# Kernel optimization log

Measured on AMD Instinct MI355X. Metric: run time of the kernel, lower is better.

Reference implementation:

```python
import jax, jax.numpy as jnp
import numpy as np

B, FIN, FOUT, FH = 32, 32, 32, 64
H = W = 128
LAT = 512
K_IN, K_MID, K_OUT, K_SHORT = FH * FIN, FH * FH, FOUT * FH, FOUT * FIN
K_TOTAL = K_IN + K_MID + K_OUT + K_SHORT + FH + FH + FOUT + FOUT  # 9408


def setup_inputs() -> dict:
    key = jax.random.key(0)
    ks = jax.random.split(key, 20)
    def rn(k, shape, scale=None):
        s = scale if scale is not None else 1.0 / np.sqrt(shape[-1])
        return jax.random.normal(k, shape, dtype=jnp.float32) * s
    return {
        "x": jax.random.normal(ks[0], (B, FIN, H, W), dtype=jnp.float32),
        "lat": jax.random.normal(ks[1], (B, LAT), dtype=jnp.float32),
        "w0": rn(ks[2], (LAT, LAT)), "b0": rn(ks[3], (LAT,), 0.02),
        "w1a": rn(ks[4], (2 * LAT, LAT)), "b1a": rn(ks[5], (2 * LAT,), 0.02),
        "w1b": rn(ks[6], (LAT, 2 * LAT)), "b1b": rn(ks[7], (LAT,), 0.02),
        "w1s": rn(ks[8], (LAT, LAT)), "b1s": rn(ks[9], (LAT,), 0.02),
        "w2a": rn(ks[10], (2 * LAT, LAT)), "b2a": rn(ks[11], (2 * LAT,), 0.02),
        "w2b": rn(ks[12], (K_TOTAL, 2 * LAT)), "b2b": rn(ks[13], (K_TOTAL,), 0.02),
        "w2s": rn(ks[14], (K_TOTAL, LAT)), "b2s": rn(ks[15], (K_TOTAL,), 0.02),
        "wfa": rn(ks[16], (K_TOTAL, K_TOTAL)), "bfa": rn(ks[17], (K_TOTAL,), 0.02),
    }


def _lrb(h, wa, ba, wb, bb, ws, bs):
    # LinearResidualBlock: shortcut + 2-layer MLP with ReLU
    return h @ ws.T + bs + jax.nn.relu(h @ wa.T + ba) @ wb.T + bb


def reference(x, lat, w0, b0, w1a, b1a, w1b, b1b, w1s, b1s,
              w2a, b2a, w2b, b2b, w2s, b2s, wfa, bfa):
    # hypernetwork: dyna_k then LinearFA (forward is a plain linear)
    h = lat @ w0.T + b0                              # [B, 512]
    h = _lrb(h, w1a, b1a, w1b, b1b, w1s, b1s)        # [B, 512]
    h = _lrb(h, w2a, b2a, w2b, b2b, w2s, b2s)        # [B, K_TOTAL]
    ks = h @ wfa.T + bfa                             # [B, K_TOTAL]

    sizes = [K_IN, K_MID, K_OUT, K_SHORT, FH, FH, FOUT, FOUT]
    offs = np.cumsum([0] + sizes)
    k_in = ks[:, offs[0]:offs[1]].reshape(B, FH, FIN)
    k_mid = ks[:, offs[1]:offs[2]].reshape(B, FH, FH)
    k_out = ks[:, offs[2]:offs[3]].reshape(B, FOUT, FH)
    k_short = ks[:, offs[3]:offs[4]].reshape(B, FOUT, FIN)
    b_in = ks[:, offs[4]:offs[5]][:, :, None, None]    # [B, FH, 1, 1]
    b_mid = ks[:, offs[5]:offs[6]][:, :, None, None]
    b_out = ks[:, offs[6]:offs[7]][:, :, None, None]   # [B, FOUT, 1, 1]
    b_short = ks[:, offs[7]:offs[8]][:, :, None, None]

    # per-sample 1x1 grouped convs == batched matmuls over channels
    xs = jnp.einsum('bihw,boi->bohw', x, k_short) + b_short
    xn = jax.nn.relu(jnp.einsum('bihw,boi->bohw', x, k_in) + b_in)
    xn = jax.nn.relu(jnp.einsum('bihw,boi->bohw', xn, k_mid) + b_mid)
    xn = jnp.einsum('bihw,boi->bohw', xn, k_out) + b_out
    return xn + xs
```

## Files before the change

### kernel.cpp

```cpp
#include <hip/hip_runtime.h>
#include <cstdint>

#define KT 9408
#define NT 256
#define KC 16

__global__ __launch_bounds__(256, 1) void gemm32_partial(
    const float* __restrict__ X1, const float* __restrict__ W1, int K1,
    const float* __restrict__ X2, const float* __restrict__ W2, int K2,
    float* __restrict__ partial, int O, int ksplit)
{
    __shared__ float Xs[KC][32];
    __shared__ float Wt[KC][NT];

    const int t      = threadIdx.x;
    const int o0     = blockIdx.x * NT;
    const int s      = blockIdx.y;
    const int kchunk = (K1 + K2) / ksplit;
    const int kbeg   = s * kchunk;
    const int kend   = kbeg + kchunk;
    const int lane   = t & 63;
    const int wv     = t >> 6;

    const int sr  = t >> 2;
    const int sc4 = (t & 3) << 2;

    float4 wpre[4];
    float  xpre[2];

    {
        int kc0 = kbeg;
#pragma unroll
        for (int p = 0; p < 4; ++p) {
            int r = sr + 64 * p;
            int o = o0 + r;
            int kg = kc0 + sc4;
            float4 v = make_float4(0.f, 0.f, 0.f, 0.f);
            if (o < O)
                v = (kg < K1) ? *(const float4*)&W1[(size_t)o * K1 + kg]
                              : *(const float4*)&W2[(size_t)o * K2 + (kg - K1)];
            wpre[p] = v;
        }
#pragma unroll
        for (int it = 0; it < 2; ++it) {
            int idx = t + 256 * it;
            int kg  = kc0 + (idx >> 5);
            int bb  = idx & 31;
            xpre[it] = (kg < K1) ? X1[(size_t)bb * K1 + kg]
                                 : X2[(size_t)bb * K2 + (kg - K1)];
        }
    }

    float acc[8][4];
#pragma unroll
    for (int bi = 0; bi < 8; bi++)
#pragma unroll
        for (int j = 0; j < 4; j++) acc[bi][j] = 0.f;

    for (int kc0 = kbeg; kc0 < kend; kc0 += KC) {
#pragma unroll
        for (int it = 0; it < 2; ++it) {
            int idx = t + 256 * it;
            Xs[idx >> 5][idx & 31] = xpre[it];
        }
#pragma unroll
        for (int p = 0; p < 4; ++p) {
            int r = sr + 64 * p;
            Wt[sc4 + 0][r] = wpre[p].x;
            Wt[sc4 + 1][r] = wpre[p].y;
            Wt[sc4 + 2][r] = wpre[p].z;
            Wt[sc4 + 3][r] = wpre[p].w;
        }
        __syncthreads();

        if (kc0 + KC < kend) {
            int kn = kc0 + KC;
#pragma unroll
            for (int p = 0; p < 4; ++p) {
                int r = sr + 64 * p;
                int o = o0 + r;
                int kg = kn + sc4;
                float4 v = make_float4(0.f, 0.f, 0.f, 0.f);
                if (o < O)
                    v = (kg < K1) ? *(const float4*)&W1[(size_t)o * K1 + kg]
                                  : *(const float4*)&W2[(size_t)o * K2 + (kg - K1)];
                wpre[p] = v;
            }
#pragma unroll
            for (int it = 0; it < 2; ++it) {
                int idx = t + 256 * it;
                int kg  = kn + (idx >> 5);
                int bb  = idx & 31;
                xpre[it] = (kg < K1) ? X1[(size_t)bb * K1 + kg]
                                     : X2[(size_t)bb * K2 + (kg - K1)];
            }
        }

#pragma unroll
        for (int c = 0; c < KC; c++) {
            float4 xa = *(const float4*)&Xs[c][wv * 8];
            float4 xb = *(const float4*)&Xs[c][wv * 8 + 4];
            float xv[8] = {xa.x, xa.y, xa.z, xa.w, xb.x, xb.y, xb.z, xb.w};
            float w[4];
#pragma unroll
            for (int j = 0; j < 4; j++) w[j] = Wt[c][lane + 64 * j];
#pragma unroll
            for (int bi = 0; bi < 8; bi++)
#pragma unroll
                for (int j = 0; j < 4; j++) acc[bi][j] += xv[bi] * w[j];
        }
        __syncthreads();
    }

#pragma unroll
    for (int bi = 0; bi < 8; bi++) {
        int b = wv * 8 + bi;
#pragma unroll
        for (int j = 0; j < 4; j++) {
            int o = o0 + lane + 64 * j;
            if (o < O)
                partial[((size_t)s * 32 + b) * O + o] = acc[bi][j];
        }
    }
}

__global__ __launch_bounds__(256) void reduce_bias(
    const float* __restrict__ partial, const float* __restrict__ bias1,
    const float* __restrict__ bias2, float* __restrict__ Y, int O, int relu,
    int ksplit)
{
    int idx = blockIdx.x * 256 + threadIdx.x;
    if (idx >= 32 * O) return;
    int b = idx / O, o = idx - b * O;
    float s = bias1[o] + (bias2 ? bias2[o] : 0.f);
    for (int k = 0; k < ksplit; k++)
        s += partial[((size_t)k * 32 + b) * O + o];
    Y[idx] = relu ? fmaxf(s, 0.f) : s;
}

typedef __attribute__((ext_vector_type(8))) short bf16x8;
typedef __attribute__((ext_vector_type(4))) float f32x4;

__device__ inline uint32_t pkbf(float lo, float hi) {
    uint32_t a = __builtin_bit_cast(uint32_t, lo);
    uint32_t b = __builtin_bit_cast(uint32_t, hi);
    a = (a + 0x7FFFu + ((a >> 16) & 1u)) >> 16;
    b = (b + 0x7FFFu + ((b >> 16) & 1u)) & 0xFFFF0000u;
    return a | b;
}

#define MFMA16(a, b, c) __builtin_amdgcn_mfma_f32_16x16x32_bf16(a, b, c, 0, 0, 0)

#define TPW 16

__global__ __launch_bounds__(256, 3) void conv_mfma(
    const float* __restrict__ x, const float* __restrict__ ks,
    float* __restrict__ out)
{
    const int t  = threadIdx.x;
    const int b  = blockIdx.y;
    const int l  = t & 63;
    const int g  = l >> 4;
    const int n  = l & 15;
    const int wid = blockIdx.x * 4 + (t >> 6);

    const float* __restrict__ kb = ks + (size_t)b * KT;

    auto loadA = [&](const float* W, int ldw, int row0, int k0) -> bf16x8 {
        const float* p = W + (size_t)(row0 + n) * ldw + k0 + 4 * g;
        float4 lo = *(const float4*)p;
        float4 hi = *(const float4*)(p + 16);
        union { bf16x8 v; uint32_t u[4]; } r;
        r.u[0] = pkbf(lo.x, lo.y);
        r.u[1] = pkbf(lo.z, lo.w);
        r.u[2] = pkbf(hi.x, hi.y);
        r.u[3] = pkbf(hi.z, hi.w);
        return r.v;
    };
    auto loadBias = [&](int off) -> f32x4 {
        float4 v = *(const float4*)&kb[off + 4 * g];
        f32x4 r; r[0] = v.x; r[1] = v.y; r[2] = v.z; r[3] = v.w;
        return r;
    };

    bf16x8 ain[4], amid[4][2], aout[2][2], ashort[2];
#pragma unroll
    for (int rt = 0; rt < 4; ++rt) ain[rt] = loadA(kb, 32, 16 * rt, 0);
#pragma unroll
    for (int ot = 0; ot < 4; ++ot)
#pragma unroll
        for (int kf = 0; kf < 2; ++kf) amid[ot][kf] = loadA(kb + 2048, 64, 16 * ot, 32 * kf);
#pragma unroll
    for (int ot = 0; ot < 2; ++ot)
#pragma unroll
        for (int kf = 0; kf < 2; ++kf) aout[ot][kf] = loadA(kb + 6144, 64, 16 * ot, 32 * kf);
#pragma unroll
    for (int ot = 0; ot < 2; ++ot) ashort[ot] = loadA(kb + 8192, 32, 16 * ot, 0);

    f32x4 bin[4], bmid[4], bos[2];
#pragma unroll
    for (int rt = 0; rt < 4; ++rt) bin[rt] = loadBias(9216 + 16 * rt);
#pragma unroll
    for (int ot = 0; ot < 4; ++ot) bmid[ot] = loadBias(9280 + 16 * ot);
#pragma unroll
    for (int ot = 0; ot < 2; ++ot) {
        f32x4 a = loadBias(9344 + 16 * ot);
        f32x4 c = loadBias(9376 + 16 * ot);
#pragma unroll
        for (int r = 0; r < 4; ++r) a[r] += c[r];
        bos[ot] = a;
    }

    const float* __restrict__ xbase = x + (size_t)b * 524288 + (size_t)(4 * g) * 16384 + n;
    float* __restrict__ obase = out + (size_t)b * 524288 + (size_t)(4 * g) * 16384 + n;

#pragma unroll 1
    for (int it = 0; it < TPW; ++it) {
        const int px0 = (wid * TPW + it) * 16;

        const float* p = xbase + px0;
        float e0 = p[0], e1 = p[16384], e2 = p[2 * 16384], e3 = p[3 * 16384];
        const float* q = p + (size_t)16 * 16384;
        float e4 = q[0], e5 = q[16384], e6 = q[2 * 16384], e7 = q[3 * 16384];
        union { bf16x8 v; uint32_t u[4]; } bx;
        bx.u[0] = pkbf(e0, e1); bx.u[1] = pkbf(e2, e3);
        bx.u[2] = pkbf(e4, e5); bx.u[3] = pkbf(e6, e7);

        f32x4 h[4];
#pragma unroll
        for (int rt = 0; rt < 4; ++rt) {
            f32x4 acc = MFMA16(ain[rt], bx.v, bin[rt]);
#pragma unroll
            for (int r = 0; r < 4; ++r) acc[r] = fmaxf(acc[r], 0.f);
            h[rt] = acc;
        }
        union { bf16x8 v; uint32_t u[4]; } hb0, hb1;
        hb0.u[0] = pkbf(h[0][0], h[0][1]); hb0.u[1] = pkbf(h[0][2], h[0][3]);
        hb0.u[2] = pkbf(h[1][0], h[1][1]); hb0.u[3] = pkbf(h[1][2], h[1][3]);
        hb1.u[0] = pkbf(h[2][0], h[2][1]); hb1.u[1] = pkbf(h[2][2], h[2][3]);
        hb1.u[2] = pkbf(h[3][0], h[3][1]); hb1.u[3] = pkbf(h[3][2], h[3][3]);

        f32x4 m[4];
#pragma unroll
        for (int ot = 0; ot < 4; ++ot) {
            f32x4 acc = MFMA16(amid[ot][0], hb0.v, bmid[ot]);
            acc = MFMA16(amid[ot][1], hb1.v, acc);
#pragma unroll
            for (int r = 0; r < 4; ++r) acc[r] = fmaxf(acc[r], 0.f);
            m[ot] = acc;
        }
        union { bf16x8 v; uint32_t u[4]; } mb0, mb1;
        mb0.u[0] = pkbf(m[0][0], m[0][1]); mb0.u[1] = pkbf(m[0][2], m[0][3]);
        mb0.u[2] = pkbf(m[1][0], m[1][1]); mb0.u[3] = pkbf(m[1][2], m[1][3]);
        mb1.u[0] = pkbf(m[2][0], m[2][1]); mb1.u[1] = pkbf(m[2][2], m[2][3]);
        mb1.u[2] = pkbf(m[3][0], m[3][1]); mb1.u[3] = pkbf(m[3][2], m[3][3]);

#pragma unroll
        for (int ot = 0; ot < 2; ++ot) {
            f32x4 acc = MFMA16(ashort[ot], bx.v, bos[ot]);
            acc = MFMA16(aout[ot][0], mb0.v, acc);
            acc = MFMA16(aout[ot][1], mb1.v, acc);
            float* po = obase + (size_t)(16 * ot) * 16384 + px0;
            po[0]         = acc[0];
            po[16384]     = acc[1];
            po[2 * 16384] = acc[2];
            po[3 * 16384] = acc[3];
        }
    }
}

extern "C" void kernel_launch(void* const* d_in, const int* in_sizes, int n_in,
                              void* d_out, int out_size, void* d_ws, size_t ws_size,
                              hipStream_t stream)
{
    const float* x   = (const float*)d_in[0];
    const float* lat = (const float*)d_in[1];
    const float* w0  = (const float*)d_in[2];
    const float* b0  = (const float*)d_in[3];
    const float* w1a = (const float*)d_in[4];
    const float* b1a = (const float*)d_in[5];
    const float* w1b = (const float*)d_in[6];
    const float* b1b = (const float*)d_in[7];
    const float* w1s = (const float*)d_in[8];
    const float* b1s = (const float*)d_in[9];
    const float* w2a = (const float*)d_in[10];
    const float* b2a = (const float*)d_in[11];
    const float* w2b = (const float*)d_in[12];
    const float* b2b = (const float*)d_in[13];
    const float* w2s = (const float*)d_in[14];
    const float* b2s = (const float*)d_in[15];
    const float* wfa = (const float*)d_in[16];
    const float* bfa = (const float*)d_in[17];

    float* ws  = (float*)d_ws;
    float* h0  = ws;
    float* t1  = ws + 16384;
    float* h1  = ws + 49152;
    float* t2  = ws + 65536;
    float* h2  = ws + 98304;
    float* ksb = ws + 399360;
    float* pbuf = (float*)d_out;

    dim3 blk(256);
    auto g  = [](int O, int ks) { return dim3((unsigned)((O + NT - 1) / NT), (unsigned)ks); };
    auto rg = [](int O) { return dim3((unsigned)((32 * O + 255) / 256)); };

    gemm32_partial<<<g(512, 32), blk, 0, stream>>>(lat, w0, 512, nullptr, nullptr, 0, pbuf, 512, 32);
    reduce_bias<<<rg(512), blk, 0, stream>>>(pbuf, b0, nullptr, h0, 512, 0, 32);
    gemm32_partial<<<g(1024, 32), blk, 0, stream>>>(h0, w1a, 512, nullptr, nullptr, 0, pbuf, 1024, 32);
    reduce_bias<<<rg(1024), blk, 0, stream>>>(pbuf, b1a, nullptr, t1, 1024, 1, 32);
    gemm32_partial<<<g(512, 32), blk, 0, stream>>>(h0, w1s, 512, t1, w1b, 1024, pbuf, 512, 32);
    reduce_bias<<<rg(512), blk, 0, stream>>>(pbuf, b1s, b1b, h1, 512, 0, 32);
    gemm32_partial<<<g(1024, 32), blk, 0, stream>>>(h1, w2a, 512, nullptr, nullptr, 0, pbuf, 1024, 32);
    reduce_bias<<<rg(1024), blk, 0, stream>>>(pbuf, b2a, nullptr, t2, 1024, 1, 32);
    gemm32_partial<<<g(KT, 32), blk, 0, stream>>>(h1, w2s, 512, t2, w2b, 1024, pbuf, KT, 32);
    reduce_bias<<<rg(KT), blk, 0, stream>>>(pbuf, b2s, b2b, h2, KT, 0, 32);
    gemm32_partial<<<g(KT, 28), blk, 0, stream>>>(h2, wfa, KT, nullptr, nullptr, 0, pbuf, KT, 28);
    reduce_bias<<<rg(KT), blk, 0, stream>>>(pbuf, bfa, nullptr, ksb, KT, 0, 28);

    conv_mfma<<<dim3(16, 32), blk, 0, stream>>>(x, ksb, (float*)d_out);
}
```

Baseline: 293.8 us.

## Replace split-K plus reduce with fused small-GEMM kernel for hypernet layers

Adds a smallgemm kernel that splits K across the four waves of one block, reduces in shared memory, and applies bias and ReLU in-kernel. This replaces the split-K gemm32_partial plus reduce_bias pairs for the first five linear layers, removing five launches and the partial-buffer round trips. The large wfa GEMM keeps the split-K path but moves from 28 to 21 splits. The small kernels launch few blocks for the 512/1024-wide layers and do not double-buffer their loads, so latency hiding may be weaker.

```diff
diff --git a/kernel.cpp b/kernel.cpp
--- a/kernel.cpp
+++ b/kernel.cpp
@@ -5,9 +5,82 @@
 #define NT 256
 #define KC 16
 
+__global__ __launch_bounds__(256) void smallgemm(
+    const float* __restrict__ X1, const float* __restrict__ W1, int K1,
+    const float* __restrict__ X2, const float* __restrict__ W2, int K2,
+    const float* __restrict__ bias1, const float* __restrict__ bias2,
+    float* __restrict__ Y, int O, int relu)
+{
+    __shared__ float Xs[4][KC][32];
+    __shared__ float Wt[4][KC][16];
+    __shared__ float red[4][16][32];
+
+    const int t    = threadIdx.x;
+    const int lane = t & 63;
+    const int w    = t >> 6;
+    const int o0   = blockIdx.x * 16;
+    const int o_l  = lane & 15;
+    const int bg   = lane >> 4;
+    const int Kq   = (K1 + K2) >> 2;
+    const int kbeg = w * Kq;
+    const int kend = kbeg + Kq;
+
+    const int wr  = lane >> 2;
+    const int wc4 = (lane & 3) << 2;
+
+    float acc[8];
+#pragma unroll
+    for (int i = 0; i < 8; ++i) acc[i] = 0.f;
+
+    for (int kc = kbeg; kc < kend; kc += KC) {
+#pragma unroll
+        for (int i = 0; i < 8; ++i) {
+            int idx = lane + 64 * i;
+            int c   = idx >> 5;
+            int bb  = idx & 31;
+            int kg  = kc + c;
+            Xs[w][c][bb] = (kg < K1) ? X1[(size_t)bb * K1 + kg]
+                                     : X2[(size_t)bb * K2 + (kg - K1)];
+        }
+        {
+            int kg = kc + wc4;
+            float4 v = (kg < K1) ? *(const float4*)&W1[(size_t)(o0 + wr) * K1 + kg]
+                                 : *(const float4*)&W2[(size_t)(o0 + wr) * K2 + (kg - K1)];
+            Wt[w][wc4 + 0][wr] = v.x;
+            Wt[w][wc4 + 1][wr] = v.y;
+            Wt[w][wc4 + 2][wr] = v.z;
+            Wt[w][wc4 + 3][wr] = v.w;
+        }
+#pragma unroll
+        for (int c = 0; c < KC; ++c) {
+            float wv = Wt[w][c][o_l];
+            float4 xa = *(const float4*)&Xs[w][c][8 * bg];
+            float4 xb = *(const float4*)&Xs[w][c][8 * bg + 4];
+            acc[0] += wv * xa.x; acc[1] += wv * xa.y;
+            acc[2] += wv * xa.z; acc[3] += wv * xa.w;
+            acc[4] += wv * xb.x; acc[5] += wv * xb.y;
+            acc[6] += wv * xb.z; acc[7] += wv * xb.w;
+        }
+    }
+
+#pragma unroll
+    for (int bi = 0; bi < 8; ++bi) red[w][o_l][8 * bg + bi] = acc[bi];
+    __syncthreads();
+
+#pragma unroll
+    for (int half = 0; half < 2; ++half) {
+        int cell = t + 256 * half;
+        int o = cell >> 5;
+        int b = cell & 31;
+        float s = red[0][o][b] + red[1][o][b] + red[2][o][b] + red[3][o][b];
+        s += bias1[o0 + o] + (bias2 ? bias2[o0 + o] : 0.f);
+        if (relu) s = fmaxf(s, 0.f);
+        Y[(size_t)b * O + o0 + o] = s;
+    }
+}
+
 __global__ __launch_bounds__(256, 1) void gemm32_partial(
     const float* __restrict__ X1, const float* __restrict__ W1, int K1,
-    const float* __restrict__ X2, const float* __restrict__ W2, int K2,
     float* __restrict__ partial, int O, int ksplit)
 {
     __shared__ float Xs[KC][32];
@@ -16,7 +89,7 @@
     const int t      = threadIdx.x;
     const int o0     = blockIdx.x * NT;
     const int s      = blockIdx.y;
-    const int kchunk = (K1 + K2) / ksplit;
+    const int kchunk = K1 / ksplit;
     const int kbeg   = s * kchunk;
     const int kend   = kbeg + kchunk;
     const int lane   = t & 63;
@@ -34,20 +107,14 @@
         for (int p = 0; p < 4; ++p) {
             int r = sr + 64 * p;
             int o = o0 + r;
-            int kg = kc0 + sc4;
             float4 v = make_float4(0.f, 0.f, 0.f, 0.f);
-            if (o < O)
-                v = (kg < K1) ? *(const float4*)&W1[(size_t)o * K1 + kg]
-                              : *(const float4*)&W2[(size_t)o * K2 + (kg - K1)];
+            if (o < O) v = *(const float4*)&W1[(size_t)o * K1 + kc0 + sc4];
             wpre[p] = v;
         }
 #pragma unroll
         for (int it = 0; it < 2; ++it) {
             int idx = t + 256 * it;
-            int kg  = kc0 + (idx >> 5);
-            int bb  = idx & 31;
-            xpre[it] = (kg < K1) ? X1[(size_t)bb * K1 + kg]
-                                 : X2[(size_t)bb * K2 + (kg - K1)];
+            xpre[it] = X1[(size_t)(idx & 31) * K1 + kc0 + (idx >> 5)];
         }
     }
 
@@ -79,20 +146,14 @@
             for (int p = 0; p < 4; ++p) {
                 int r = sr + 64 * p;
                 int o = o0 + r;
-                int kg = kn + sc4;
                 float4 v = make_float4(0.f, 0.f, 0.f, 0.f);
-                if (o < O)
-                    v = (kg < K1) ? *(const float4*)&W1[(size_t)o * K1 + kg]
-                                  : *(const float4*)&W2[(size_t)o * K2 + (kg - K1)];
+                if (o < O) v = *(const float4*)&W1[(size_t)o * K1 + kn + sc4];
                 wpre[p] = v;
             }
 #pragma unroll
             for (int it = 0; it < 2; ++it) {
                 int idx = t + 256 * it;
-                int kg  = kn + (idx >> 5);
-                int bb  = idx & 31;
-                xpre[it] = (kg < K1) ? X1[(size_t)bb * K1 + kg]
-                                     : X2[(size_t)bb * K2 + (kg - K1)];
+                xpre[it] = X1[(size_t)(idx & 31) * K1 + kn + (idx >> 5)];
             }
         }
 
@@ -101,13 +162,13 @@
             float4 xa = *(const float4*)&Xs[c][wv * 8];
             float4 xb = *(const float4*)&Xs[c][wv * 8 + 4];
             float xv[8] = {xa.x, xa.y, xa.z, xa.w, xb.x, xb.y, xb.z, xb.w};
-            float w[4];
-#pragma unroll
-            for (int j = 0; j < 4; j++) w[j] = Wt[c][lane + 64 * j];
+            float ww[4];
+#pragma unroll
+            for (int j = 0; j < 4; j++) ww[j] = Wt[c][lane + 64 * j];
 #pragma unroll
             for (int bi = 0; bi < 8; bi++)
 #pragma unroll
-                for (int j = 0; j < 4; j++) acc[bi][j] += xv[bi] * w[j];
+                for (int j = 0; j < 4; j++) acc[bi][j] += xv[bi] * ww[j];
         }
         __syncthreads();
     }
@@ -126,16 +187,15 @@
 
 __global__ __launch_bounds__(256) void reduce_bias(
     const float* __restrict__ partial, const float* __restrict__ bias1,
-    const float* __restrict__ bias2, float* __restrict__ Y, int O, int relu,
-    int ksplit)
+    float* __restrict__ Y, int O, int ksplit)
 {
     int idx = blockIdx.x * 256 + threadIdx.x;
     if (idx >= 32 * O) return;
     int b = idx / O, o = idx - b * O;
-    float s = bias1[o] + (bias2 ? bias2[o] : 0.f);
+    float s = bias1[o];
     for (int k = 0; k < ksplit; k++)
         s += partial[((size_t)k * 32 + b) * O + o];
-    Y[idx] = relu ? fmaxf(s, 0.f) : s;
+    Y[idx] = s;
 }
 
 typedef __attribute__((ext_vector_type(8))) short bf16x8;
@@ -302,21 +362,19 @@
     float* pbuf = (float*)d_out;
 
     dim3 blk(256);
-    auto g  = [](int O, int ks) { return dim3((unsigned)((O + NT - 1) / NT), (unsigned)ks); };
-    auto rg = [](int O) { return dim3((unsigned)((32 * O + 255) / 256)); };
-
-    gemm32_partial<<<g(512, 32), blk, 0, stream>>>(lat, w0, 512, nullptr, nullptr, 0, pbuf, 512, 32);
-    reduce_bias<<<rg(512), blk, 0, stream>>>(pbuf, b0, nullptr, h0, 512, 0, 32);
-    gemm32_partial<<<g(1024, 32), blk, 0, stream>>>(h0, w1a, 512, nullptr, nullptr, 0, pbuf, 1024, 32);
-    reduce_bias<<<rg(1024), blk, 0, stream>>>(pbuf, b1a, nullptr, t1, 1024, 1, 32);
-    gemm32_partial<<<g(512, 32), blk, 0, stream>>>(h0, w1s, 512, t1, w1b, 1024, pbuf, 512, 32);
-    reduce_bias<<<rg(512), blk, 0, stream>>>(pbuf, b1s, b1b, h1, 512, 0, 32);
-    gemm32_partial<<<g(1024, 32), blk, 0, stream>>>(h1, w2a, 512, nullptr, nullptr, 0, pbuf, 1024, 32);
-    reduce_bias<<<rg(1024), blk, 0, stream>>>(pbuf, b2a, nullptr, t2, 1024, 1, 32);
-    gemm32_partial<<<g(KT, 32), blk, 0, stream>>>(h1, w2s, 512, t2, w2b, 1024, pbuf, KT, 32);
-    reduce_bias<<<rg(KT), blk, 0, stream>>>(pbuf, b2s, b2b, h2, KT, 0, 32);
-    gemm32_partial<<<g(KT, 28), blk, 0, stream>>>(h2, wfa, KT, nullptr, nullptr, 0, pbuf, KT, 28);
-    reduce_bias<<<rg(KT), blk, 0, stream>>>(pbuf, bfa, nullptr, ksb, KT, 0, 28);
+
+    smallgemm<<<dim3(32), blk, 0, stream>>>(lat, w0, 512, nullptr, nullptr, 0,
+                                            b0, nullptr, h0, 512, 0);
+    smallgemm<<<dim3(64), blk, 0, stream>>>(h0, w1a, 512, nullptr, nullptr, 0,
+                                            b1a, nullptr, t1, 1024, 1);
+    smallgemm<<<dim3(32), blk, 0, stream>>>(h0, w1s, 512, t1, w1b, 1024,
+                                            b1s, b1b, h1, 512, 0);
+    smallgemm<<<dim3(64), blk, 0, stream>>>(h1, w2a, 512, nullptr, nullptr, 0,
+                                            b2a, nullptr, t2, 1024, 1);
+    smallgemm<<<dim3(588), blk, 0, stream>>>(h1, w2s, 512, t2, w2b, 1024,
+                                             b2s, b2b, h2, KT, 0);
+    gemm32_partial<<<dim3(37, 21), blk, 0, stream>>>(h2, wfa, KT, pbuf, KT, 21);
+    reduce_bias<<<dim3((32 * KT + 255) / 256), blk, 0, stream>>>(pbuf, bfa, ksb, KT, 21);
 
     conv_mfma<<<dim3(16, 32), blk, 0, stream>>>(x, ksb, (float*)d_out);
 }
```

New measurement: 338.6 us. +15.2%, slower.
